# Performance work log

Measured on AMD Instinct MI355X. Metric: run time of the kernel, lower is better.

The kernel has to match this reference:

```python
import jax, jax.numpy as jnp
import numpy as np

B, T, N, F = 32, 64, 128, 128
U, K1, K2 = 64, 64, 32
EPS = 1e-3  # keras BatchNormalization default epsilon
SLOPE = 0.01  # LeakyReLU negative_slope


def setup_inputs() -> dict:
    key = jax.random.key(0)
    ks = jax.random.split(key, 16)
    g = lambda k, sh, s=0.05: jax.random.normal(k, sh, dtype=jnp.float32) * s
    inp = {
        "x": jax.random.normal(ks[0], (B, T, F), dtype=jnp.float32),
        "a": jax.random.uniform(ks[1], (B, N, N), dtype=jnp.float32),
        # LSTM (keras gate order i, f, c, o)
        "lstm_k": g(ks[2], (F, 4 * U)),
        "lstm_r": g(ks[3], (U, 4 * U)),
        "lstm_b": jnp.zeros((4 * U,), jnp.float32),
        # BatchNorm params (inference form: gamma, beta, moving mean, moving var)
        "bnl_g": jnp.ones((U,), jnp.float32), "bnl_b": jnp.zeros((U,), jnp.float32),
        "bnl_m": jnp.zeros((U,), jnp.float32), "bnl_v": jnp.ones((U,), jnp.float32),
        "w1": g(ks[4], (U, K1)), "b1": jnp.zeros((K1,), jnp.float32),
        "bn1_g": jnp.ones((K1,), jnp.float32), "bn1_b": jnp.zeros((K1,), jnp.float32),
        "bn1_m": jnp.zeros((K1,), jnp.float32), "bn1_v": jnp.ones((K1,), jnp.float32),
        "w2": g(ks[5], (K1, K2)), "b2": jnp.zeros((K2,), jnp.float32),
        "bn2_g": jnp.ones((K2,), jnp.float32), "bn2_b": jnp.zeros((K2,), jnp.float32),
        "bn2_m": jnp.zeros((K2,), jnp.float32), "bn2_v": jnp.ones((K2,), jnp.float32),
        "d1_w": g(ks[6], (T * N * K2, 3), 0.01), "d1_b": jnp.zeros((3,), jnp.float32),
        "d2_w": g(ks[7], (3, N)), "d2_b": jnp.zeros((N,), jnp.float32),
    }
    return inp


def _bn(x, g, b, m, v):
    return (x - m) * (g * jax.lax.rsqrt(v + EPS)) + b


def _leaky(x):
    return jnp.where(x >= 0, x, SLOPE * x)


def _lstm(x, Wk, Wr, b):
    # x: [B, T, F] -> hs: [B, T, U]
    xz = jnp.einsum('btf,fg->btg', x, Wk) + b  # precompute input projections
    u = Wr.shape[0]
    h0 = jnp.zeros((x.shape[0], u), x.dtype)
    c0 = jnp.zeros((x.shape[0], u), x.dtype)

    def step(carry, zt):
        h, c = carry
        z = zt + h @ Wr
        i, f, g_, o = jnp.split(z, 4, axis=-1)
        i = jax.nn.sigmoid(i); f = jax.nn.sigmoid(f)
        g_ = jnp.tanh(g_); o = jax.nn.sigmoid(o)
        c = f * c + i * g_
        h = o * jnp.tanh(c)
        return (h, c), h

    _, hs = jax.lax.scan(step, (h0, c0), xz.transpose(1, 0, 2))
    return hs.transpose(1, 0, 2)


def reference(x, a, lstm_k, lstm_r, lstm_b, bnl_g, bnl_b, bnl_m, bnl_v,
              w1, b1, bn1_g, bn1_b, bn1_m, bn1_v,
              w2, b2, bn2_g, bn2_b, bn2_m, bn2_v,
              d1_w, d1_b, d2_w, d2_b):
    h = _lstm(x, lstm_k, lstm_r, lstm_b)              # [B, T, U]
    h = _bn(h, bnl_g, bnl_b, bnl_m, bnl_v)            # inference BN; dropout is identity
    # tile each timestep's LSTM output over the N nodes, then GCN1
    support1 = jnp.einsum('btu,uk->btk', h, w1)       # [B, T, K1] (identical across nodes)
    sup1 = jnp.broadcast_to(support1[:, :, None, :], (h.shape[0], h.shape[1], N, w1.shape[1]))
    g1 = jnp.einsum('bij,btjk->btik', a, sup1) + b1   # adjacency matmul
    g1 = _leaky(g1)
    g1 = _bn(g1, bn1_g, bn1_b, bn1_m, bn1_v)
    # GCN2
    sup2 = jnp.einsum('btnk,km->btnm', g1, w2)
    g2 = jnp.einsum('bij,btjm->btim', a, sup2) + b2
    g2 = _leaky(g2)
    g2 = _bn(g2, bn2_g, bn2_b, bn2_m, bn2_v)          # [B, T, N, K2]
    flat = g2.reshape(g2.shape[0], -1)                # [B, T*N*K2]
    d1 = jax.nn.relu(flat @ d1_w + d1_b)              # [B, 3]
    return d1 @ d2_w + d2_b                           # [B, N]
```

## Files before the change

### kernel.cpp

```cpp
#include <hip/hip_runtime.h>

#define BB 32
#define TT 64
#define NN 128
#define FF 128
#define UU 64
#define K1 64
#define K2 32
#define G4 256
#define EPSV 1e-3f
#define SLOPE 0.01f

#define ALD 136
#define SLD 136
#define WLD 72

typedef __attribute__((ext_vector_type(8))) short short8;
typedef __attribute__((ext_vector_type(4))) float f32x4;
typedef __attribute__((ext_vector_type(2))) __fp16 half2v;

__device__ __forceinline__ float sigmoidf_(float x) {
  return __builtin_amdgcn_rcpf(1.f + __expf(-x));
}
__device__ __forceinline__ float tanhf_(float x) {
  return 1.f - 2.f * __builtin_amdgcn_rcpf(__expf(2.f * x) + 1.f);
}
__device__ __forceinline__ float leaky_(float x) { return x >= 0.f ? x : SLOPE * x; }
__device__ __forceinline__ unsigned short f2bf(float x) {
  union { float f; unsigned u; } v; v.f = x;
  unsigned r = v.u + 0x7fff + ((v.u >> 16) & 1);
  return (unsigned short)(r >> 16);
}

__global__ __launch_bounds__(256) void k_xzp(const float* __restrict__ x,
                                             const float* __restrict__ wk,
                                             const float* __restrict__ bias,
                                             const float* __restrict__ wr,
                                             const float* __restrict__ w1,
                                             float* __restrict__ xz,
                                             unsigned* __restrict__ wrp,
                                             unsigned* __restrict__ w1p) {
  int tid = threadIdx.x;
  if (blockIdx.x < 256) {
    __shared__ float xs[8][FF];
    int row0 = blockIdx.x * 8;
    for (int i = tid; i < 8 * FF; i += 256) xs[i >> 7][i & 127] = x[(size_t)row0 * FF + i];
    __syncthreads();
    int g = tid;
    float acc[8];
    float bg = bias[g];
#pragma unroll
    for (int r = 0; r < 8; ++r) acc[r] = bg;
    for (int f = 0; f < FF; ++f) {
      float w = wk[f * G4 + g];
#pragma unroll
      for (int r = 0; r < 8; ++r) acc[r] += xs[r][f] * w;
    }
#pragma unroll
    for (int r = 0; r < 8; ++r) xz[(size_t)(row0 + r) * G4 + g] = acc[r];
  } else if (blockIdx.x == 256) {
    for (int idx = tid; idx < 4 * 32 * UU; idx += 256) {
      int p = idx & 31;
      int gate = (idx >> 5) & 3;
      int u = idx >> 7;
      int col = gate * UU + u;
      union { __fp16 h[2]; unsigned u; } pk;
      pk.h[0] = (__fp16)wr[(2 * p) * G4 + col];
      pk.h[1] = (__fp16)wr[(2 * p + 1) * G4 + col];
      wrp[idx] = pk.u;
    }
  } else {
    for (int idx = tid; idx < 32 * K1; idx += 256) {
      int p = idx & 31, k = idx >> 5;
      union { __fp16 h[2]; unsigned u; } pk;
      pk.h[0] = (__fp16)w1[(2 * p) * K1 + k];
      pk.h[1] = (__fp16)w1[(2 * p + 1) * K1 + k];
      w1p[idx] = pk.u;
    }
  }
}

__global__ __launch_bounds__(256, 1) void k_mega(
    const float* __restrict__ xz, const unsigned* __restrict__ wrp,
    const unsigned* __restrict__ w1p,
    const float* __restrict__ bnl_g, const float* __restrict__ bnl_b,
    const float* __restrict__ bnl_m, const float* __restrict__ bnl_v,
    const float* __restrict__ a, const float* __restrict__ w2,
    const float* __restrict__ d1w,
    float* __restrict__ s1out, float* __restrict__ rsum,
    unsigned short* __restrict__ apad, unsigned short* __restrict__ w2t,
    float4* __restrict__ d1r) {
  __shared__ __align__(16) char smem[76032];
  int tid = threadIdx.x;
  int blk = blockIdx.x;

  if (blk < 32) {
    float* xz_lds = (float*)smem;
    __fp16* hp = (__fp16*)(smem + 65536);
    float* zex = (float*)(smem + 73728);
    __fp16* h16 = (__fp16*)(smem + 75776);
    int wave = tid >> 6, lane = tid & 63;
    int role = wave & 1;
    int b = blk;

    {
      const float4* src = (const float4*)(xz + (size_t)b * TT * G4);
      float4* dst = (float4*)xz_lds;
#pragma unroll
      for (int k = 0; k < 16; ++k) dst[tid + k * 256] = src[tid + k * 256];
    }
    unsigned wv0[32], wv1[32];
    if (wave < 2) {
      const uint4* wp = (const uint4*)(wrp + (size_t)lane * 128 + role * 64);
#pragma unroll
      for (int k = 0; k < 8; ++k) {
        uint4 v = wp[k];
        wv0[4 * k + 0] = v.x; wv0[4 * k + 1] = v.y; wv0[4 * k + 2] = v.z; wv0[4 * k + 3] = v.w;
      }
#pragma unroll
      for (int k = 0; k < 8; ++k) {
        uint4 v = wp[8 + k];
        wv1[4 * k + 0] = v.x; wv1[4 * k + 1] = v.y; wv1[4 * k + 2] = v.z; wv1[4 * k + 3] = v.w;
      }
      h16[wave * UU + lane] = (__fp16)0.f;
    }
    float bscale = bnl_g[lane] * rsqrtf(bnl_v[lane] + EPSV);
    float boff = bnl_b[lane] - bnl_m[lane] * bscale;
    float c = 0.f;
    __syncthreads();

    for (int t = 0; t < TT; ++t) {
      int par = t & 1;
      float z0, z1;
      if (wave < 2) {
        unsigned hw[32];
        const uint4* hq = (const uint4*)(h16 + wave * UU);
#pragma unroll
        for (int k = 0; k < 8; ++k) {
          uint4 v = hq[k];
          hw[4 * k + 0] = v.x; hw[4 * k + 1] = v.y; hw[4 * k + 2] = v.z; hw[4 * k + 3] = v.w;
        }
        z0 = xz_lds[t * G4 + role * 128 + lane];
        z1 = xz_lds[t * G4 + role * 128 + 64 + lane];
#pragma unroll
        for (int p = 0; p < 32; ++p) {
          half2v hh = __builtin_bit_cast(half2v, hw[p]);
          z0 = __builtin_amdgcn_fdot2(__builtin_bit_cast(half2v, wv0[p]), hh, z0, false);
          z1 = __builtin_amdgcn_fdot2(__builtin_bit_cast(half2v, wv1[p]), hh, z1, false);
        }
        zex[(par * 2 + role) * 128 + lane] = z0;
        zex[(par * 2 + role) * 128 + 64 + lane] = z1;
      }
      __syncthreads();
      if (wave < 2) {
        float pz0 = zex[(par * 2 + (role ^ 1)) * 128 + lane];
        float pz1 = zex[(par * 2 + (role ^ 1)) * 128 + 64 + lane];
        float zi = role ? pz0 : z0;
        float zf = role ? pz1 : z1;
        float zg = role ? z0 : pz0;
        float zo = role ? z1 : pz1;
        float i_ = sigmoidf_(zi), f_ = sigmoidf_(zf), g_ = tanhf_(zg), o_ = sigmoidf_(zo);
        c = f_ * c + i_ * g_;
        float h = o_ * tanhf_(c);
        h16[wave * UU + lane] = (__fp16)h;
        if (role == 0) hp[t * UU + lane] = (__fp16)(h * bscale + boff);
      }
    }
    __syncthreads();

    unsigned w1v[32];
    {
      const uint4* wp1 = (const uint4*)(w1p + (size_t)lane * 32);
#pragma unroll
      for (int k = 0; k < 8; ++k) {
        uint4 v = wp1[k];
        w1v[4 * k + 0] = v.x; w1v[4 * k + 1] = v.y; w1v[4 * k + 2] = v.z; w1v[4 * k + 3] = v.w;
      }
    }
    float* s1b = s1out + (size_t)b * TT * K1;
    for (int r = 0; r < 16; ++r) {
      int t = wave * 16 + r;
      unsigned hw2[32];
      const uint4* hq = (const uint4*)(hp + t * UU);
#pragma unroll
      for (int k = 0; k < 8; ++k) {
        uint4 v = hq[k];
        hw2[4 * k + 0] = v.x; hw2[4 * k + 1] = v.y; hw2[4 * k + 2] = v.z; hw2[4 * k + 3] = v.w;
      }
      float acc = 0.f;
#pragma unroll
      for (int p = 0; p < 32; ++p)
        acc = __builtin_amdgcn_fdot2(__builtin_bit_cast(half2v, w1v[p]),
                                     __builtin_bit_cast(half2v, hw2[p]), acc, false);
      s1b[t * K1 + lane] = acc;
    }
  } else if (blk < 64) {
    int b = blk - 32;
    int wave = tid >> 6, lane = tid & 63;
    const float* ab = a + (size_t)b * NN * NN;
    for (int r = 0; r < 32; ++r) {
      int row = wave * 32 + r;
      float2 v = *(const float2*)(ab + (size_t)row * NN + lane * 2);
      float s = v.x + v.y;
#pragma unroll
      for (int off = 32; off >= 1; off >>= 1) s += __shfl_down(s, off);
      if (lane == 0) rsum[b * NN + row] = s;
    }
    unsigned short* ap = apad + (size_t)b * NN * ALD;
    for (int idx = tid; idx < NN * NN; idx += 256) {
      int i = idx >> 7, j = idx & 127;
      ap[i * ALD + j] = f2bf(ab[idx]);
    }
  } else if (blk == 64) {
    for (int idx = tid; idx < K1 * K2; idx += 256) {
      int k = idx >> 5, m = idx & 31;
      w2t[m * WLD + k] = f2bf(w2[idx]);
    }
  } else {
    int t = blk - 65;
    float* dt = (float*)smem;
    const float* src = d1w + (size_t)t * NN * K2 * 3;
    for (int c32 = 0; c32 < 4; ++c32) {
      __syncthreads();
      for (int i = tid; i < 768; i += 256)
        ((float4*)dt)[i] = ((const float4*)(src + c32 * 3072))[i];
      __syncthreads();
#pragma unroll
      for (int q = 0; q < 3; ++q) {
        int item = q * 256 + tid;
        int l = item & 63;
        int gc = item >> 6;
        int g = gc / 3, cc = gc % 3;
        int it = g >> 1, mt = g & 1;
        int l15v = l & 15, l4v = l >> 4;
        int m = mt * 16 + l15v;
        int rowbase = it * 16 + l4v * 4;
        float4 v;
        v.x = dt[(rowbase + 0) * 96 + m * 3 + cc];
        v.y = dt[(rowbase + 1) * 96 + m * 3 + cc];
        v.z = dt[(rowbase + 2) * 96 + m * 3 + cc];
        v.w = dt[(rowbase + 3) * 96 + m * 3 + cc];
        d1r[(((size_t)t * 4 + g) * 3 + cc) * 256 + c32 * 64 + l] = v;
      }
    }
  }
}

__global__ __launch_bounds__(256) void k_gcn(
    const float* __restrict__ s1g, const float* __restrict__ rsum,
    const unsigned short* __restrict__ apad, const unsigned short* __restrict__ w2t,
    const float* __restrict__ b1,
    const float* __restrict__ bn1_g, const float* __restrict__ bn1_b,
    const float* __restrict__ bn1_m, const float* __restrict__ bn1_v,
    const float* __restrict__ b2,
    const float* __restrict__ bn2_g, const float* __restrict__ bn2_b,
    const float* __restrict__ bn2_m, const float* __restrict__ bn2_v,
    const float4* __restrict__ d1r, float* __restrict__ part) {
  __shared__ unsigned short a_lds[NN * ALD];
  __shared__ unsigned short s2_lds[K2 * SLD];
  __shared__ unsigned short w2_lds[K2 * WLD];
  __shared__ float4 gp[K1];
  __shared__ float r_lds[NN];
  __shared__ float p2[3 * K2];
  __shared__ float red[12];

  int blk = blockIdx.x;
  int b = blk & 31, t = blk >> 5;
  int tid = threadIdx.x;
  int lane = tid & 63, wave = tid >> 6;
  int l15 = lane & 15, l4 = lane >> 4;

  {
    const uint4* src = (const uint4*)(apad + (size_t)b * NN * ALD);
    uint4* dst = (uint4*)a_lds;
    for (int i = tid; i < NN * ALD / 8; i += 256) dst[i] = src[i];
  }
  {
    const uint2* src = (const uint2*)w2t;
    uint2* dst = (uint2*)w2_lds;
    for (int i = tid; i < K2 * WLD / 4; i += 256) dst[i] = src[i];
  }
  if (tid < K1) {
    float s1v = s1g[((size_t)b * TT + t) * K1 + tid];
    float s = bn1_g[tid] * rsqrtf(bn1_v[tid] + EPSV);
    gp[tid] = make_float4(s1v, b1[tid], s, bn1_b[tid] - bn1_m[tid] * s);
  }
  if (tid >= 64 && tid < 64 + NN) r_lds[tid - 64] = rsum[b * NN + (tid - 64)];
  if (tid >= 192 && tid < 192 + K2) {
    int m = tid - 192;
    float s = bn2_g[m] * rsqrtf(bn2_v[m] + EPSV);
    p2[m] = b2[m];
    p2[K2 + m] = s;
    p2[2 * K2 + m] = bn2_b[m] - bn2_m[m] * s;
  }
  __syncthreads();

  f32x4 z4 = {0.f, 0.f, 0.f, 0.f};

  {
    float rj0 = r_lds[(wave * 2 + 0) * 16 + l15];
    float rj1 = r_lds[(wave * 2 + 1) * 16 + l15];
    f32x4 acc[2][2];
    acc[0][0] = z4; acc[0][1] = z4; acc[1][0] = z4; acc[1][1] = z4;
#pragma unroll
    for (int kt = 0; kt < 2; ++kt) {
      float4 gpv[8];
#pragma unroll
      for (int e = 0; e < 8; ++e) gpv[e] = gp[kt * 32 + l4 * 8 + e];
      short8 bfrag0 = *((const short8*)&w2_lds[(0 + l15) * WLD + kt * 32 + l4 * 8]);
      short8 bfrag1 = *((const short8*)&w2_lds[(16 + l15) * WLD + kt * 32 + l4 * 8]);
#pragma unroll
      for (int jt = 0; jt < 2; ++jt) {
        float rj = jt ? rj1 : rj0;
        short8 af;
#pragma unroll
        for (int e = 0; e < 8; ++e) {
          float4 p = gpv[e];
          float v = leaky_(rj * p.x + p.y) * p.z + p.w;
          af[e] = (short)f2bf(v);
        }
        acc[jt][0] = __builtin_amdgcn_mfma_f32_16x16x32_bf16(af, bfrag0, acc[jt][0], 0, 0, 0);
        acc[jt][1] = __builtin_amdgcn_mfma_f32_16x16x32_bf16(af, bfrag1, acc[jt][1], 0, 0, 0);
      }
    }
#pragma unroll
    for (int jt = 0; jt < 2; ++jt) {
      int jbase = (wave * 2 + jt) * 16 + l4 * 4;
#pragma unroll
      for (int mt = 0; mt < 2; ++mt) {
        int m = mt * 16 + l15;
        unsigned lo = (unsigned)f2bf(acc[jt][mt][0]) | ((unsigned)f2bf(acc[jt][mt][1]) << 16);
        unsigned hi = (unsigned)f2bf(acc[jt][mt][2]) | ((unsigned)f2bf(acc[jt][mt][3]) << 16);
        uint2 val; val.x = lo; val.y = hi;
        *((uint2*)&s2_lds[m * SLD + jbase]) = val;
      }
    }
  }
  __syncthreads();

  float c0 = 0.f, c1 = 0.f, c2 = 0.f;
  {
    f32x4 acc[2][2];
    acc[0][0] = z4; acc[0][1] = z4; acc[1][0] = z4; acc[1][1] = z4;
#pragma unroll
    for (int kt = 0; kt < 4; ++kt) {
      short8 bfrag0 = *((const short8*)&s2_lds[(0 + l15) * SLD + kt * 32 + l4 * 8]);
      short8 bfrag1 = *((const short8*)&s2_lds[(16 + l15) * SLD + kt * 32 + l4 * 8]);
#pragma unroll
      for (int it = 0; it < 2; ++it) {
        int i = (wave * 2 + it) * 16 + l15;
        short8 afrag = *((const short8*)&a_lds[i * ALD + kt * 32 + l4 * 8]);
        acc[it][0] = __builtin_amdgcn_mfma_f32_16x16x32_bf16(afrag, bfrag0, acc[it][0], 0, 0, 0);
        acc[it][1] = __builtin_amdgcn_mfma_f32_16x16x32_bf16(afrag, bfrag1, acc[it][1], 0, 0, 0);
      }
    }
    float gv[2][2][4];
#pragma unroll
    for (int it = 0; it < 2; ++it)
#pragma unroll
      for (int mt = 0; mt < 2; ++mt) {
        int m = mt * 16 + l15;
        float bb = p2[m], bs = p2[K2 + m], bo = p2[2 * K2 + m];
#pragma unroll
        for (int r = 0; r < 4; ++r) gv[it][mt][r] = leaky_(acc[it][mt][r] + bb) * bs + bo;
      }
#pragma unroll
    for (int g = 0; g < 4; ++g) {
      int it = g >> 1, mt = g & 1;
      float4 v0 = d1r[(((size_t)t * 4 + g) * 3 + 0) * 256 + tid];
      float4 v1 = d1r[(((size_t)t * 4 + g) * 3 + 1) * 256 + tid];
      float4 v2 = d1r[(((size_t)t * 4 + g) * 3 + 2) * 256 + tid];
      c0 += gv[it][mt][0] * v0.x + gv[it][mt][1] * v0.y + gv[it][mt][2] * v0.z + gv[it][mt][3] * v0.w;
      c1 += gv[it][mt][0] * v1.x + gv[it][mt][1] * v1.y + gv[it][mt][2] * v1.z + gv[it][mt][3] * v1.w;
      c2 += gv[it][mt][0] * v2.x + gv[it][mt][1] * v2.y + gv[it][mt][2] * v2.z + gv[it][mt][3] * v2.w;
    }
  }
#pragma unroll
  for (int off = 32; off >= 1; off >>= 1) {
    c0 += __shfl_down(c0, off);
    c1 += __shfl_down(c1, off);
    c2 += __shfl_down(c2, off);
  }
  if (lane == 0) { red[wave * 3 + 0] = c0; red[wave * 3 + 1] = c1; red[wave * 3 + 2] = c2; }
  __syncthreads();
  if (tid == 0) {
    float s0 = 0.f, s1v = 0.f, s2v = 0.f;
    for (int w = 0; w < 4; ++w) { s0 += red[w * 3]; s1v += red[w * 3 + 1]; s2v += red[w * 3 + 2]; }
    part[((size_t)b * TT + t) * 3 + 0] = s0;
    part[((size_t)b * TT + t) * 3 + 1] = s1v;
    part[((size_t)b * TT + t) * 3 + 2] = s2v;
  }
}

__global__ __launch_bounds__(128) void k_out(const float* __restrict__ part,
                                             const float* __restrict__ d1b,
                                             const float* __restrict__ d2w,
                                             const float* __restrict__ d2b,
                                             float* __restrict__ out) {
  int b = blockIdx.x, n = threadIdx.x;
  float s[3] = {0.f, 0.f, 0.f};
  const float* p = part + (size_t)b * TT * 3;
  for (int t = 0; t < TT; ++t) {
    s[0] += p[t * 3];
    s[1] += p[t * 3 + 1];
    s[2] += p[t * 3 + 2];
  }
  float o = d2b[n];
#pragma unroll
  for (int c = 0; c < 3; ++c) {
    float d = s[c] + d1b[c];
    d = d > 0.f ? d : 0.f;
    o += d * d2w[c * NN + n];
  }
  out[b * NN + n] = o;
}

extern "C" void kernel_launch(void* const* d_in, const int* in_sizes, int n_in,
                              void* d_out, int out_size, void* d_ws, size_t ws_size,
                              hipStream_t stream) {
  const float* x      = (const float*)d_in[0];
  const float* a      = (const float*)d_in[1];
  const float* lstm_k = (const float*)d_in[2];
  const float* lstm_r = (const float*)d_in[3];
  const float* lstm_b = (const float*)d_in[4];
  const float* bnl_g  = (const float*)d_in[5];
  const float* bnl_b  = (const float*)d_in[6];
  const float* bnl_m  = (const float*)d_in[7];
  const float* bnl_v  = (const float*)d_in[8];
  const float* w1     = (const float*)d_in[9];
  const float* b1     = (const float*)d_in[10];
  const float* bn1_g  = (const float*)d_in[11];
  const float* bn1_b  = (const float*)d_in[12];
  const float* bn1_m  = (const float*)d_in[13];
  const float* bn1_v  = (const float*)d_in[14];
  const float* w2     = (const float*)d_in[15];
  const float* b2     = (const float*)d_in[16];
  const float* bn2_g  = (const float*)d_in[17];
  const float* bn2_b  = (const float*)d_in[18];
  const float* bn2_m  = (const float*)d_in[19];
  const float* bn2_v  = (const float*)d_in[20];
  const float* d1_w   = (const float*)d_in[21];
  const float* d1_b   = (const float*)d_in[22];
  const float* d2_w   = (const float*)d_in[23];
  const float* d2_b   = (const float*)d_in[24];
  float* out = (float*)d_out;

  char* ws = (char*)d_ws;
  float* xz            = (float*)(ws + 0);
  float* s1            = (float*)(ws + 2097152);
  float* rsum          = (float*)(ws + 2621440);
  float* part          = (float*)(ws + 2637824);
  unsigned short* apad = (unsigned short*)(ws + 2662400);
  unsigned short* w2t  = (unsigned short*)(ws + 3776512);
  unsigned* wrp        = (unsigned*)(ws + 3781120);
  unsigned* w1p        = (unsigned*)(ws + 3813888);
  float4* d1r          = (float4*)(ws + 3822080);

  k_xzp<<<258, 256, 0, stream>>>(x, lstm_k, lstm_b, lstm_r, w1, xz, wrp, w1p);
  k_mega<<<129, 256, 0, stream>>>(xz, wrp, w1p, bnl_g, bnl_b, bnl_m, bnl_v,
                                  a, w2, d1_w, s1, rsum, apad, w2t, d1r);
  k_gcn<<<BB * TT, 256, 0, stream>>>(s1, rsum, apad, w2t, b1, bn1_g, bn1_b, bn1_m, bn1_v,
                                     b2, bn2_g, bn2_b, bn2_m, bn2_v, d1r, part);
  k_out<<<BB, 128, 0, stream>>>(part, d1_b, d2_w, d2_b, out);
}
```

Measured before the change: 72.31 us.

## Process two timesteps per GCN block to reuse staged adjacency and weights

Each k_gcn block now handles two consecutive timesteps for the same batch. The 128x128 adjacency tile and W2 are loaded into LDS once and reused across both steps, and the block count is halved. This cuts repeated global-to-LDS staging of the adjacency matrix, at the cost of a serial loop with extra barriers and less parallelism per launch. The partial sums and k_out are resized to 32 groups, and sched_barriers are added around the LSTM recurrence step to constrain instruction scheduling.

```diff
diff --git a/kernel.cpp b/kernel.cpp
--- a/kernel.cpp
+++ b/kernel.cpp
@@ -133,6 +133,7 @@
       int par = t & 1;
       float z0, z1;
       if (wave < 2) {
+        __builtin_amdgcn_sched_barrier(0);
         unsigned hw[32];
         const uint4* hq = (const uint4*)(h16 + wave * UU);
 #pragma unroll
@@ -163,6 +164,7 @@
         c = f_ * c + i_ * g_;
         float h = o_ * tanhf_(c);
         h16[wave * UU + lane] = (__fp16)h;
+        __builtin_amdgcn_sched_barrier(0);
         if (role == 0) hp[t * UU + lane] = (__fp16)(h * bscale + boff);
       }
     }
@@ -259,13 +261,15 @@
   __shared__ unsigned short a_lds[NN * ALD];
   __shared__ unsigned short s2_lds[K2 * SLD];
   __shared__ unsigned short w2_lds[K2 * WLD];
+  __shared__ float s1l[2][K1];
   __shared__ float4 gp[K1];
   __shared__ float r_lds[NN];
   __shared__ float p2[3 * K2];
   __shared__ float red[12];
 
   int blk = blockIdx.x;
-  int b = blk & 31, t = blk >> 5;
+  int b = blk & 31, tg = blk >> 5;
+  int t0 = tg * 2;
   int tid = threadIdx.x;
   int lane = tid & 63, wave = tid >> 6;
   int l15 = lane & 15, l4 = lane >> 4;
@@ -280,12 +284,12 @@
     uint2* dst = (uint2*)w2_lds;
     for (int i = tid; i < K2 * WLD / 4; i += 256) dst[i] = src[i];
   }
+  if (tid < 128) ((float*)s1l)[tid] = s1g[((size_t)b * TT + t0) * K1 + tid];
   if (tid < K1) {
-    float s1v = s1g[((size_t)b * TT + t) * K1 + tid];
     float s = bn1_g[tid] * rsqrtf(bn1_v[tid] + EPSV);
-    gp[tid] = make_float4(s1v, b1[tid], s, bn1_b[tid] - bn1_m[tid] * s);
-  }
-  if (tid >= 64 && tid < 64 + NN) r_lds[tid - 64] = rsum[b * NN + (tid - 64)];
+    gp[tid] = make_float4(b1[tid], s, bn1_b[tid] - bn1_m[tid] * s, 0.f);
+  }
+  if (tid >= 64 && tid < 192) r_lds[tid - 64] = rsum[b * NN + (tid - 64)];
   if (tid >= 192 && tid < 192 + K2) {
     int m = tid - 192;
     float s = bn2_g[m] * rsqrtf(bn2_v[m] + EPSV);
@@ -296,19 +300,30 @@
   __syncthreads();
 
   f32x4 z4 = {0.f, 0.f, 0.f, 0.f};
-
-  {
-    float rj0 = r_lds[(wave * 2 + 0) * 16 + l15];
-    float rj1 = r_lds[(wave * 2 + 1) * 16 + l15];
-    f32x4 acc[2][2];
-    acc[0][0] = z4; acc[0][1] = z4; acc[1][0] = z4; acc[1][1] = z4;
+  float rj0 = r_lds[(wave * 2 + 0) * 16 + l15];
+  float rj1 = r_lds[(wave * 2 + 1) * 16 + l15];
+  short8 bw[2][2];
+#pragma unroll
+  for (int kt = 0; kt < 2; ++kt) {
+    bw[kt][0] = *((const short8*)&w2_lds[(0 + l15) * WLD + kt * 32 + l4 * 8]);
+    bw[kt][1] = *((const short8*)&w2_lds[(16 + l15) * WLD + kt * 32 + l4 * 8]);
+  }
+
+  float c0 = 0.f, c1 = 0.f, c2 = 0.f;
+
+  for (int ti = 0; ti < 2; ++ti) {
+    int t = t0 + ti;
+    f32x4 a1[2][2];
+    a1[0][0] = z4; a1[0][1] = z4; a1[1][0] = z4; a1[1][1] = z4;
 #pragma unroll
     for (int kt = 0; kt < 2; ++kt) {
       float4 gpv[8];
-#pragma unroll
-      for (int e = 0; e < 8; ++e) gpv[e] = gp[kt * 32 + l4 * 8 + e];
-      short8 bfrag0 = *((const short8*)&w2_lds[(0 + l15) * WLD + kt * 32 + l4 * 8]);
-      short8 bfrag1 = *((const short8*)&w2_lds[(16 + l15) * WLD + kt * 32 + l4 * 8]);
+      float s1v[8];
+#pragma unroll
+      for (int e = 0; e < 8; ++e) {
+        gpv[e] = gp[kt * 32 + l4 * 8 + e];
+        s1v[e] = s1l[ti][kt * 32 + l4 * 8 + e];
+      }
 #pragma unroll
       for (int jt = 0; jt < 2; ++jt) {
         float rj = jt ? rj1 : rj0;
@@ -316,30 +331,28 @@
 #pragma unroll
         for (int e = 0; e < 8; ++e) {
           float4 p = gpv[e];
-          float v = leaky_(rj * p.x + p.y) * p.z + p.w;
+          float v = leaky_(rj * s1v[e] + p.x) * p.y + p.z;
           af[e] = (short)f2bf(v);
         }
-        acc[jt][0] = __builtin_amdgcn_mfma_f32_16x16x32_bf16(af, bfrag0, acc[jt][0], 0, 0, 0);
-        acc[jt][1] = __builtin_amdgcn_mfma_f32_16x16x32_bf16(af, bfrag1, acc[jt][1], 0, 0, 0);
-      }
-    }
+        a1[jt][0] = __builtin_amdgcn_mfma_f32_16x16x32_bf16(af, bw[kt][0], a1[jt][0], 0, 0, 0);
+        a1[jt][1] = __builtin_amdgcn_mfma_f32_16x16x32_bf16(af, bw[kt][1], a1[jt][1], 0, 0, 0);
+      }
+    }
+    __syncthreads();
 #pragma unroll
     for (int jt = 0; jt < 2; ++jt) {
       int jbase = (wave * 2 + jt) * 16 + l4 * 4;
 #pragma unroll
       for (int mt = 0; mt < 2; ++mt) {
         int m = mt * 16 + l15;
-        unsigned lo = (unsigned)f2bf(acc[jt][mt][0]) | ((unsigned)f2bf(acc[jt][mt][1]) << 16);
-        unsigned hi = (unsigned)f2bf(acc[jt][mt][2]) | ((unsigned)f2bf(acc[jt][mt][3]) << 16);
+        unsigned lo = (unsigned)f2bf(a1[jt][mt][0]) | ((unsigned)f2bf(a1[jt][mt][1]) << 16);
+        unsigned hi = (unsigned)f2bf(a1[jt][mt][2]) | ((unsigned)f2bf(a1[jt][mt][3]) << 16);
         uint2 val; val.x = lo; val.y = hi;
         *((uint2*)&s2_lds[m * SLD + jbase]) = val;
       }
     }
-  }
-  __syncthreads();
-
-  float c0 = 0.f, c1 = 0.f, c2 = 0.f;
-  {
+    __syncthreads();
+
     f32x4 acc[2][2];
     acc[0][0] = z4; acc[0][1] = z4; acc[1][0] = z4; acc[1][1] = z4;
 #pragma unroll
@@ -375,6 +388,7 @@
       c2 += gv[it][mt][0] * v2.x + gv[it][mt][1] * v2.y + gv[it][mt][2] * v2.z + gv[it][mt][3] * v2.w;
     }
   }
+
 #pragma unroll
   for (int off = 32; off >= 1; off >>= 1) {
     c0 += __shfl_down(c0, off);
@@ -386,9 +400,9 @@
   if (tid == 0) {
     float s0 = 0.f, s1v = 0.f, s2v = 0.f;
     for (int w = 0; w < 4; ++w) { s0 += red[w * 3]; s1v += red[w * 3 + 1]; s2v += red[w * 3 + 2]; }
-    part[((size_t)b * TT + t) * 3 + 0] = s0;
-    part[((size_t)b * TT + t) * 3 + 1] = s1v;
-    part[((size_t)b * TT + t) * 3 + 2] = s2v;
+    part[((size_t)b * 32 + tg) * 3 + 0] = s0;
+    part[((size_t)b * 32 + tg) * 3 + 1] = s1v;
+    part[((size_t)b * 32 + tg) * 3 + 2] = s2v;
   }
 }
 
@@ -399,11 +413,12 @@
                                              float* __restrict__ out) {
   int b = blockIdx.x, n = threadIdx.x;
   float s[3] = {0.f, 0.f, 0.f};
-  const float* p = part + (size_t)b * TT * 3;
-  for (int t = 0; t < TT; ++t) {
-    s[0] += p[t * 3];
-    s[1] += p[t * 3 + 1];
-    s[2] += p[t * 3 + 2];
+  const float* p = part + (size_t)b * 32 * 3;
+#pragma unroll
+  for (int g = 0; g < 32; ++g) {
+    s[0] += p[g * 3];
+    s[1] += p[g * 3 + 1];
+    s[2] += p[g * 3 + 2];
   }
   float o = d2b[n];
 #pragma unroll
@@ -459,7 +474,7 @@
   k_xzp<<<258, 256, 0, stream>>>(x, lstm_k, lstm_b, lstm_r, w1, xz, wrp, w1p);
   k_mega<<<129, 256, 0, stream>>>(xz, wrp, w1p, bnl_g, bnl_b, bnl_m, bnl_v,
                                   a, w2, d1_w, s1, rsum, apad, w2t, d1r);
-  k_gcn<<<BB * TT, 256, 0, stream>>>(s1, rsum, apad, w2t, b1, bn1_g, bn1_b, bn1_m, bn1_v,
-                                     b2, bn2_g, bn2_b, bn2_m, bn2_v, d1r, part);
+  k_gcn<<<1024, 256, 0, stream>>>(s1, rsum, apad, w2t, b1, bn1_g, bn1_b, bn1_m, bn1_v,
+                                  b2, bn2_g, bn2_b, bn2_m, bn2_v, d1r, part);
   k_out<<<BB, 128, 0, stream>>>(part, d1_b, d2_w, d2_b, out);
 }
```

Result: no change. 71.79 us, median of 2 (-0.7%).
